# Kernel optimization log

Measured on AMD Instinct MI355X. Metric: run time of the kernel, lower is better.

Reference implementation:

```python
import jax, jax.numpy as jnp
import numpy as np

N, IN_DIM, HID = 8192, 256, 512
NEG_INF = jnp.float32(-1e30)


def _linear_params(key, fan_in, fan_out):
    k1, k2 = jax.random.split(key)
    bound = 1.0 / np.sqrt(fan_in)
    W = jax.random.uniform(k1, (fan_in, fan_out), jnp.float32, -bound, bound)
    b = jax.random.uniform(k2, (fan_out,), jnp.float32, -bound, bound)
    return W, b


def setup_inputs() -> dict:
    key = jax.random.key(0)
    ks = jax.random.split(key, 10)
    x = jax.random.normal(ks[0], (N, IN_DIM), jnp.float32)
    adj = jax.random.randint(ks[1], (N, N), 0, 2) > 0
    adj = adj | jnp.eye(N, dtype=bool)  # self-loops: no all-masked rows
    Win, b_in = _linear_params(ks[2], IN_DIM, HID)
    Wq, bq = _linear_params(ks[3], HID, HID)
    Wk, bk = _linear_params(ks[4], HID, HID)
    Wv, bv = _linear_params(ks[5], HID, HID)
    Wo, bo = _linear_params(ks[6], HID, HID)
    Ws, bs = _linear_params(ks[7], HID, 1)
    Wf1, bf1 = _linear_params(ks[8], HID, HID)
    Wf2, bf2 = _linear_params(ks[9], HID, HID)
    g1 = jnp.ones((HID,), jnp.float32); be1 = jnp.zeros((HID,), jnp.float32)
    g2 = jnp.ones((HID,), jnp.float32); be2 = jnp.zeros((HID,), jnp.float32)
    return dict(x=x, adj=adj, Win=Win, b_in=b_in, Wq=Wq, bq=bq, Wk=Wk, bk=bk,
                Wv=Wv, bv=bv, Wo=Wo, bo=bo, Ws=Ws, bs=bs,
                g1=g1, be1=be1, g2=g2, be2=be2,
                Wf1=Wf1, bf1=bf1, Wf2=Wf2, bf2=bf2)


def _layernorm(x, g, b, eps=1e-5):
    mu = jnp.mean(x, axis=-1, keepdims=True)
    var = jnp.mean(jnp.square(x - mu), axis=-1, keepdims=True)
    return (x - mu) * jax.lax.rsqrt(var + eps) * g + b


def reference(x, adj, Win, b_in, Wq, bq, Wk, bk, Wv, bv, Wo, bo, Ws, bs,
              g1, be1, g2, be2, Wf1, bf1, Wf2, bf2):
    h = x @ Win + b_in                      # [N, HID]
    q = h @ Wq + bq
    k = h @ Wk + bk
    v = h @ Wv + bv
    scale = 1.0 / np.sqrt(HID).astype(np.float32)
    scores = (q @ k.T) * scale              # [N, N]
    scores = jnp.where(adj, scores, NEG_INF)
    attn = jax.nn.softmax(scores, axis=-1)  # dropout = identity (eval mode)
    h2 = attn @ v                           # [N, HID]
    h = _layernorm(h + (h2 @ Wo + bo), g1, be1)
    ff = jnp.maximum(h @ Wf1 + bf1, 0.0) @ Wf2 + bf2
    h = _layernorm(h + ff, g2, be2)
    logits = (h @ Ws + bs).squeeze(-1)      # [N]
    return logits
```

## Files before the change

### kernel.cpp

```cpp
#include <hip/hip_runtime.h>

typedef unsigned int u32;
typedef unsigned short u16;
typedef unsigned char u8;

typedef __bf16 bf16_t;
typedef bf16_t bf16x8 __attribute__((ext_vector_type(8)));
typedef float f32x4 __attribute__((ext_vector_type(4)));

#define NROW 8192
#define HID 512
#define DIN 256
#define LDQ 1536
#define NSPLIT 4
#define KVCH (NROW / NSPLIT)
#define KVB 32

__device__ __forceinline__ u16 f2b(float f) {
    u32 u = __float_as_uint(f);
    u32 r = (u + 0x7fffu + ((u >> 16) & 1u)) >> 16;
    return (u16)r;
}
__device__ __forceinline__ float b2f(u16 h) {
    return __uint_as_float(((u32)h) << 16);
}
__device__ __forceinline__ f32x4 zero4() {
    f32x4 z = {0.f, 0.f, 0.f, 0.f};
    return z;
}
__device__ __forceinline__ void gll16(const void* g, void* l) {
    __builtin_amdgcn_global_load_lds(
        (const __attribute__((address_space(1))) unsigned int*)g,
        (__attribute__((address_space(3))) unsigned int*)l, 16, 0, 0);
}

__global__ void sniff_and_bias(const u32* __restrict__ adj, int* __restrict__ mode,
                               const float* __restrict__ bq, const float* __restrict__ bk,
                               const float* __restrict__ bv, float* __restrict__ bqkv) {
    __shared__ int f01[4], ff32[4], fbf[4];
    int t = threadIdx.x, lane = t & 63, wv = t >> 6;
    for (int i = t; i < 1536; i += 256)
        bqkv[i] = i < 512 ? bq[i] : (i < 1024 ? bk[i - 512] : bv[i - 1024]);
    int all01 = 1, allf32 = 1, allbf = 1;
    for (int i = t; i < 1024; i += 256) {
        u32 w = adj[i];
        if (w > 1u) all01 = 0;
        if (w != 0u && w != 0x3f800000u) allf32 = 0;
    }
    const u16* h = (const u16*)adj;
    for (int i = t; i < 2048; i += 256) {
        u16 v = h[i];
        if (v != 0 && v != 0x3f80u) allbf = 0;
    }
    all01 = __all(all01);
    allf32 = __all(allf32);
    allbf = __all(allbf);
    if (lane == 0) { f01[wv] = all01; ff32[wv] = allf32; fbf[wv] = allbf; }
    __syncthreads();
    if (t == 0) {
        int a = f01[0] & f01[1] & f01[2] & f01[3];
        int b = ff32[0] & ff32[1] & ff32[2] & ff32[3];
        int c = fbf[0] & fbf[1] & fbf[2] & fbf[3];
        mode[0] = a ? 0 : (b ? 1 : (c ? 2 : 3));
    }
}

__global__ __launch_bounds__(256) void build_bits(const void* __restrict__ adj,
                                                  const int* __restrict__ mode,
                                                  u32* __restrict__ bits) {
    int row = blockIdx.x;
    int t = threadIdx.x;
    int lane = t & 63, wv = t >> 6;
    int md = *mode;
    for (int c0 = 0; c0 < NROW; c0 += 256) {
        int c = c0 + t;
        size_t idx = (size_t)row * NROW + c;
        bool nz;
        if (md == 0)      nz = ((const u32*)adj)[idx] != 0u;
        else if (md == 1) nz = ((const float*)adj)[idx] != 0.f;
        else if (md == 2) nz = ((const u16*)adj)[idx] != 0;
        else              nz = ((const u8*)adj)[idx] != 0;
        unsigned long long bm = __ballot(nz);
        if (lane == 0) {
            int w = row * 256 + (c0 >> 5) + wv * 2;
            bits[w] = (u32)bm;
            bits[w + 1] = (u32)(bm >> 32);
        }
    }
}

__global__ __launch_bounds__(256) void prep(const float* __restrict__ x,
                                            const float* __restrict__ Win,
                                            const float* __restrict__ Wq,
                                            const float* __restrict__ Wk,
                                            const float* __restrict__ Wv,
                                            const float* __restrict__ Wo,
                                            const float* __restrict__ Wf1,
                                            const float* __restrict__ Wf2,
                                            u16* __restrict__ pX16,
                                            u16* __restrict__ pWinT,
                                            u16* __restrict__ pQKVT,
                                            u16* __restrict__ pWoT,
                                            u16* __restrict__ pWf1T,
                                            u16* __restrict__ pWf2T) {
    int z = blockIdx.z;
    int t = threadIdx.x;
    if (z == 7) {
        size_t base = ((size_t)blockIdx.y * 8 + blockIdx.x) * 32768;
#pragma unroll 4
        for (int k = 0; k < 128; k++) {
            size_t i = base + k * 256 + t;
            pX16[i] = f2b(x[i]);
        }
        return;
    }
    const float* src;
    u16* dst;
    int R = 512;
    switch (z) {
        case 0: src = Win; dst = pWinT; R = 256; break;
        case 1: src = Wq;  dst = pQKVT; break;
        case 2: src = Wk;  dst = pQKVT + 512 * 512; break;
        case 3: src = Wv;  dst = pQKVT + 2 * 512 * 512; break;
        case 4: src = Wo;  dst = pWoT; break;
        case 5: src = Wf1; dst = pWf1T; break;
        default: src = Wf2; dst = pWf2T; break;
    }
    int r0 = blockIdx.y * 64, c0 = blockIdx.x * 64;
    if (r0 >= R) return;
    __shared__ u16 tile[64][65];
#pragma unroll
    for (int i = 0; i < 16; i++) {
        int idx = t + i * 256;
        int rr = idx >> 6, cc = idx & 63;
        tile[rr][cc] = f2b(src[(size_t)(r0 + rr) * 512 + c0 + cc]);
    }
    __syncthreads();
#pragma unroll
    for (int i = 0; i < 16; i++) {
        int idx = t + i * 256;
        int rr = idx >> 6, cc = idx & 63;
        dst[(size_t)(c0 + rr) * R + r0 + cc] = tile[cc][rr];
    }
}

__global__ __launch_bounds__(256) void transpose_v_tiled(const u16* __restrict__ in, int ldv,
                                                         u16* __restrict__ out) {
    __shared__ u16 tl[64][72];
    int c0 = blockIdx.x * 64;
    int r0 = blockIdx.y * 64;
    int t = threadIdx.x;
#pragma unroll
    for (int i = 0; i < 2; i++) {
        int idx = t + i * 256;
        int rr = idx >> 3, ck = idx & 7;
        bf16x8 v = *(const bf16x8*)(in + (size_t)(r0 + rr) * ldv + c0 + ck * 8);
#pragma unroll
        for (int j = 0; j < 8; j++) tl[ck * 8 + j][rr] = ((u16*)&v)[j];
    }
    __syncthreads();
#pragma unroll
    for (int i = 0; i < 2; i++) {
        int idx = t + i * 256;
        int col = idx >> 3, ch = idx & 7;
        int kv = ch * 8;
        bf16x8 v;
#pragma unroll
        for (int j = 0; j < 8; j++) ((u16*)&v)[j] = tl[col][kv + j];
        *(bf16x8*)(out + (size_t)((r0 + kv) >> 5) * (HID * 32) +
                   (size_t)(c0 + col) * 32 + (kv & 31)) = v;
    }
}

__global__ __launch_bounds__(256, 3) void gemm_k(const u16* __restrict__ A, int lda,
                                                 const u16* __restrict__ Bt,
                                                 const float* __restrict__ bias,
                                                 const float* __restrict__ resid,
                                                 float* __restrict__ outF,
                                                 u16* __restrict__ outH, int ldo,
                                                 int relu, int K) {
    __shared__ u16 Ald[2][8192];
    __shared__ u16 Bld[2][4096];
    int t = threadIdx.x;
    int lane = t & 63, wave = t >> 6;
    int l15 = lane & 15, lg = lane >> 4;
    int row0 = blockIdx.y * 128, col0 = blockIdx.x * 64;

    auto stage = [&](int buf, int kk) {
#pragma unroll
        for (int p = 0; p < 4; p++) {
            int idx = p * 256 + t;
            int row = idx >> 3, c = idx & 7;
            gll16(A + (size_t)(row0 + row) * lda + kk + ((c ^ (row & 7)) * 8),
                  &Ald[buf][idx * 8]);
        }
#pragma unroll
        for (int p = 0; p < 2; p++) {
            int idx = p * 256 + t;
            int row = idx >> 3, c = idx & 7;
            gll16(Bt + (size_t)(col0 + row) * K + kk + ((c ^ (row & 7)) * 8),
                  &Bld[buf][idx * 8]);
        }
    };

    f32x4 acc[2][4];
#pragma unroll
    for (int i = 0; i < 2; i++)
#pragma unroll
        for (int j = 0; j < 4; j++) acc[i][j] = zero4();

    stage(0, 0);
    asm volatile("s_waitcnt vmcnt(0)" ::: "memory");
    __syncthreads();

    int nk = K >> 6;
    for (int kt = 0; kt < nk; kt++) {
        int buf = kt & 1;
        if (kt + 1 < nk) stage(buf ^ 1, (kt + 1) * 64);
#pragma unroll
        for (int ks = 0; ks < 2; ks++) {
            bf16x8 af[2], bfr[4];
#pragma unroll
            for (int i = 0; i < 2; i++) {
                int row = wave * 32 + i * 16 + l15;
                af[i] = *(const bf16x8*)&Ald[buf][row * 64 + (((ks * 4 + lg) ^ (row & 7)) * 8)];
            }
#pragma unroll
            for (int j = 0; j < 4; j++) {
                int row = j * 16 + l15;
                bfr[j] = *(const bf16x8*)&Bld[buf][row * 64 + (((ks * 4 + lg) ^ (row & 7)) * 8)];
            }
            __builtin_amdgcn_s_setprio(1);
#pragma unroll
            for (int i = 0; i < 2; i++)
#pragma unroll
                for (int j = 0; j < 4; j++)
                    acc[i][j] = __builtin_amdgcn_mfma_f32_16x16x32_bf16(af[i], bfr[j],
                                                                       acc[i][j], 0, 0, 0);
            __builtin_amdgcn_s_setprio(0);
        }
        asm volatile("s_waitcnt vmcnt(0)" ::: "memory");
        __syncthreads();
    }
#pragma unroll
    for (int j = 0; j < 4; j++) {
        int col = col0 + j * 16 + l15;
        float bv = bias[col];
#pragma unroll
        for (int i = 0; i < 2; i++) {
#pragma unroll
            for (int r = 0; r < 4; r++) {
                int row = row0 + wave * 32 + i * 16 + lg * 4 + r;
                float v = acc[i][j][r] + bv;
                if (relu) v = fmaxf(v, 0.f);
                size_t o = (size_t)row * ldo + col;
                if (resid) v += resid[o];
                if (outF) outF[o] = v;
                if (outH) outH[o] = f2b(v);
            }
        }
    }
}

__global__ __launch_bounds__(256, 2) void attn_kernel(const u16* __restrict__ QKV,
                                                      const u16* __restrict__ VTt,
                                                      const u32* __restrict__ bits,
                                                      u16* __restrict__ Opart,
                                                      float* __restrict__ Mpart,
                                                      float* __restrict__ Lpart) {
    extern __shared__ char smem[];
    u16* Klds = (u16*)smem;
    u16* Plds = (u16*)(smem + 65536);
    float* cscL = (float*)(smem + 69632);
    int* flagsL = (int*)(smem + 69888);
    int lane = threadIdx.x & 63, wave = threadIdx.x >> 6;
    int l15 = lane & 15, lg = lane >> 4;
    int s = blockIdx.x & 3;
    int qb = blockIdx.x >> 2;
    int qrow0 = qb * 64;
    int myrows = qrow0 + wave * 16;
    const u16* Kg = QKV + 512;

    bf16x8 qf[16];
    {
        const u16* qp = QKV + (size_t)(myrows + l15) * LDQ + lg * 8;
#pragma unroll
        for (int ks = 0; ks < 16; ks++) qf[ks] = *(const bf16x8*)(qp + ks * 32);
    }

    f32x4 acc[4][8];
#pragma unroll
    for (int i = 0; i < 4; i++)
#pragma unroll
        for (int j = 0; j < 8; j++) acc[i][j] = zero4();
    float m[4] = {-1e30f, -1e30f, -1e30f, -1e30f};
    float lsum[4] = {0.f, 0.f, 0.f, 0.f};
    const float scale = 0.04419417382415922f;
    int kvbeg = s * KVCH;

    auto STAGE = [&](int buf, int kv0) {
#pragma unroll
        for (int i = 0; i < 8; i++) {
            int seg = wave * 8 + i;
            int ks = seg >> 1, q = seg & 1;
            gll16(Kg + (size_t)(kv0 + q * 16 + l15) * LDQ + ks * 32 + lg * 8,
                  Klds + buf * 16384 + seg * 512 + lane * 8);
        }
    };

    STAGE(0, kvbeg);
    asm volatile("s_waitcnt vmcnt(0)" ::: "memory");
    __syncthreads();

    const int NT = KVCH / KVB;
    for (int t = 0; t < NT; ++t) {
        int kv0 = kvbeg + t * KVB;
        int buf = t & 1;
        const u16* kb = Klds + buf * 16384;

        f32x4 sf[2];
        sf[0] = zero4(); sf[1] = zero4();
        __builtin_amdgcn_s_setprio(1);
#pragma unroll
        for (int ks = 0; ks < 16; ks++) {
            bf16x8 b0 = *(const bf16x8*)(kb + (ks * 2) * 512 + lane * 8);
            bf16x8 b1 = *(const bf16x8*)(kb + (ks * 2 + 1) * 512 + lane * 8);
            sf[0] = __builtin_amdgcn_mfma_f32_16x16x32_bf16(qf[ks], b0, sf[0], 0, 0, 0);
            sf[1] = __builtin_amdgcn_mfma_f32_16x16x32_bf16(qf[ks], b1, sf[1], 0, 0, 0);
        }
        __builtin_amdgcn_s_setprio(0);

        u32 w0[4];
#pragma unroll
        for (int r = 0; r < 4; r++)
            w0[r] = bits[(size_t)(myrows + lg * 4 + r) * 256 + (kv0 >> 5)];
        float pvv[2][4];
        float mx[4] = {-1e30f, -1e30f, -1e30f, -1e30f};
#pragma unroll
        for (int f = 0; f < 2; f++) {
            int c = f * 16 + l15;
#pragma unroll
            for (int r = 0; r < 4; r++) {
                bool bit = (w0[r] >> c) & 1u;
                float sv = bit ? sf[f][r] * scale : -1e30f;
                pvv[f][r] = sv;
                mx[r] = fmaxf(mx[r], sv);
            }
        }
        bool need = false;
#pragma unroll
        for (int r = 0; r < 4; r++) need |= (mx[r] > m[r] + 8.0f);
        int wneed = __any(need ? 1 : 0);
        float cscv[4] = {1.f, 1.f, 1.f, 1.f};
        if (wneed) {
#pragma unroll
            for (int r = 0; r < 4; r++) {
#pragma unroll
                for (int off = 8; off; off >>= 1)
                    mx[r] = fmaxf(mx[r], __shfl_xor(mx[r], off, 64));
                float mn = fmaxf(m[r], mx[r]);
                cscv[r] = __expf(m[r] - mn);
                m[r] = mn;
                lsum[r] *= cscv[r];
            }
        }
        if (l15 == 0) *(f32x4*)&cscL[wave * 16 + lg * 4] = *(f32x4*)cscv;
        if (lane == 0) flagsL[wave] = wneed;

#pragma unroll
        for (int f = 0; f < 2; f++)
#pragma unroll
            for (int r = 0; r < 4; r++)
                pvv[f][r] = (pvv[f][r] < -1e29f) ? 0.f : __expf(pvv[f][r] - m[r]);
#pragma unroll
        for (int r = 0; r < 4; r++)
            lsum[r] += pvv[0][r] + pvv[1][r];

#pragma unroll
        for (int f = 0; f < 2; f++)
#pragma unroll
            for (int r = 0; r < 4; r++)
                Plds[wave * 512 + (f * 2 + (l15 >> 3)) * 128 + (lg * 4 + r) * 8 + (l15 & 7)] =
                    f2b(pvv[f][r]);

        asm volatile("s_waitcnt lgkmcnt(0)" ::: "memory");
        __builtin_amdgcn_sched_barrier(0);
        __builtin_amdgcn_s_barrier();
        __builtin_amdgcn_sched_barrier(0);

        if (t + 1 < NT) STAGE(buf ^ 1, kv0 + KVB);

        int anyf = __any(flagsL[lane & 3] != 0);
        if (anyf) {
#pragma unroll
            for (int rf = 0; rf < 4; rf++) {
                f32x4 cs = *(const f32x4*)&cscL[rf * 16 + lg * 4];
#pragma unroll
                for (int cf = 0; cf < 8; cf++) {
                    f32x4 a = acc[rf][cf];
                    a[0] *= cs[0]; a[1] *= cs[1]; a[2] *= cs[2]; a[3] *= cs[3];
                    acc[rf][cf] = a;
                }
            }
        }

#pragma unroll
        for (int g2 = 0; g2 < 2; g2++) {
            const u16* vb = VTt + (size_t)(kv0 >> 5) * (HID * 32) +
                            (size_t)(wave * 128 + g2 * 64) * 32;
            bf16x8 vv[4];
#pragma unroll
            for (int c4 = 0; c4 < 4; c4++)
                vv[c4] = *(const bf16x8*)(vb + (size_t)(c4 * 16 + l15) * 32 + lg * 8);
            __builtin_amdgcn_s_setprio(1);
#pragma unroll
            for (int rf = 0; rf < 4; rf++) {
                bf16x8 pa = *(const bf16x8*)(Plds + rf * 512 + lane * 8);
#pragma unroll
                for (int c4 = 0; c4 < 4; c4++)
                    acc[rf][g2 * 4 + c4] = __builtin_amdgcn_mfma_f32_16x16x32_bf16(
                        pa, vv[c4], acc[rf][g2 * 4 + c4], 0, 0, 0);
            }
            __builtin_amdgcn_s_setprio(0);
        }

        asm volatile("s_waitcnt vmcnt(0) lgkmcnt(0)" ::: "memory");
        __builtin_amdgcn_sched_barrier(0);
        __builtin_amdgcn_s_barrier();
        __builtin_amdgcn_sched_barrier(0);
    }

#pragma unroll
    for (int r = 0; r < 4; r++) {
#pragma unroll
        for (int off = 8; off; off >>= 1)
            lsum[r] += __shfl_xor(lsum[r], off, 64);
    }
    if (l15 == 0) {
#pragma unroll
        for (int r = 0; r < 4; r++) {
            size_t o = (size_t)s * NROW + myrows + lg * 4 + r;
            Mpart[o] = m[r];
            Lpart[o] = lsum[r];
        }
    }
#pragma unroll
    for (int rf = 0; rf < 4; rf++)
#pragma unroll
        for (int cf = 0; cf < 8; cf++) {
            int col = wave * 128 + cf * 16 + l15;
#pragma unroll
            for (int j = 0; j < 4; j++) {
                size_t row = (size_t)s * NROW + qrow0 + rf * 16 + lg * 4 + j;
                Opart[row * HID + col] = f2b(acc[rf][cf][j]);
            }
        }
}

__global__ __launch_bounds__(256) void attn_combine(const u16* __restrict__ Opart,
                                                    const float* __restrict__ Mpart,
                                                    const float* __restrict__ Lpart,
                                                    u16* __restrict__ O16) {
    int idx = blockIdx.x * 256 + threadIdx.x;
    int row = idx >> 6;
    int c8 = (idx & 63) << 3;
    float ms[NSPLIT], M = -1e30f;
#pragma unroll
    for (int s = 0; s < NSPLIT; s++) {
        ms[s] = Mpart[(size_t)s * NROW + row];
        M = fmaxf(M, ms[s]);
    }
    float w[NSPLIT], L = 0.f;
#pragma unroll
    for (int s = 0; s < NSPLIT; s++) {
        w[s] = __expf(ms[s] - M);
        L += Lpart[(size_t)s * NROW + row] * w[s];
    }
    float inv = 1.f / L;
    float o[8];
#pragma unroll
    for (int j = 0; j < 8; j++) o[j] = 0.f;
#pragma unroll
    for (int s = 0; s < NSPLIT; s++) {
        bf16x8 p = *(const bf16x8*)(Opart + ((size_t)s * NROW + row) * HID + c8);
#pragma unroll
        for (int j = 0; j < 8; j++) o[j] += (float)p[j] * w[s];
    }
    bf16x8 res;
#pragma unroll
    for (int j = 0; j < 8; j++) {
        u16 b = f2b(o[j] * inv);
        res[j] = *(bf16_t*)&b;
    }
    *(bf16x8*)(O16 + (size_t)row * HID + c8) = res;
}

__global__ __launch_bounds__(256) void ln_single(const float* __restrict__ a,
                                                 const float* __restrict__ g,
                                                 const float* __restrict__ be,
                                                 float* __restrict__ outF,
                                                 u16* __restrict__ outH) {
    int row = blockIdx.x, t = threadIdx.x;
    const float* ar = a + (size_t)row * HID;
    float x0 = ar[t];
    float x1 = ar[t + 256];
    float s = x0 + x1, s2 = x0 * x0 + x1 * x1;
#pragma unroll
    for (int off = 32; off; off >>= 1) {
        s += __shfl_xor(s, off, 64);
        s2 += __shfl_xor(s2, off, 64);
    }
    __shared__ float ls[4], ls2[4];
    int wv = t >> 6, ln = t & 63;
    if (ln == 0) { ls[wv] = s; ls2[wv] = s2; }
    __syncthreads();
    float S = ls[0] + ls[1] + ls[2] + ls[3];
    float S2 = ls2[0] + ls2[1] + ls2[2] + ls2[3];
    float mu = S * (1.f / 512.f);
    float var = S2 * (1.f / 512.f) - mu * mu;
    float inv = rsqrtf(var + 1e-5f);
    float y0 = (x0 - mu) * inv * g[t] + be[t];
    float y1 = (x1 - mu) * inv * g[t + 256] + be[t + 256];
    size_t o = (size_t)row * HID + t;
    outF[o] = y0; outF[o + 256] = y1;
    outH[o] = f2b(y0); outH[o + 256] = f2b(y1);
}

__global__ __launch_bounds__(256) void ln_logits(const float* __restrict__ a,
                                                 const float* __restrict__ g,
                                                 const float* __restrict__ be,
                                                 const float* __restrict__ Ws,
                                                 const float* __restrict__ bs,
                                                 float* __restrict__ out) {
    int row = blockIdx.x, t = threadIdx.x;
    const float* ar = a + (size_t)row * HID;
    float x0 = ar[t];
    float x1 = ar[t + 256];
    float s = x0 + x1, s2 = x0 * x0 + x1 * x1;
#pragma unroll
    for (int off = 32; off; off >>= 1) {
        s += __shfl_xor(s, off, 64);
        s2 += __shfl_xor(s2, off, 64);
    }
    __shared__ float ls[4], ls2[4], lp[4];
    int wv = t >> 6, ln = t & 63;
    if (ln == 0) { ls[wv] = s; ls2[wv] = s2; }
    __syncthreads();
    float S = ls[0] + ls[1] + ls[2] + ls[3];
    float S2 = ls2[0] + ls2[1] + ls2[2] + ls2[3];
    float mu = S * (1.f / 512.f);
    float var = S2 * (1.f / 512.f) - mu * mu;
    float inv = rsqrtf(var + 1e-5f);
    float y0 = (x0 - mu) * inv * g[t] + be[t];
    float y1 = (x1 - mu) * inv * g[t + 256] + be[t + 256];
    float p = y0 * Ws[t] + y1 * Ws[t + 256];
#pragma unroll
    for (int off = 32; off; off >>= 1) p += __shfl_xor(p, off, 64);
    if (ln == 0) lp[wv] = p;
    __syncthreads();
    if (t == 0) out[row] = lp[0] + lp[1] + lp[2] + lp[3] + bs[0];
}

extern "C" void kernel_launch(void* const* d_in, const int* in_sizes, int n_in,
                              void* d_out, int out_size, void* d_ws, size_t ws_size,
                              hipStream_t stream) {
    const float* x   = (const float*)d_in[0];
    const void*  adj = d_in[1];
    const float* Win = (const float*)d_in[2];
    const float* b_in= (const float*)d_in[3];
    const float* Wq  = (const float*)d_in[4];
    const float* bq  = (const float*)d_in[5];
    const float* Wk  = (const float*)d_in[6];
    const float* bk  = (const float*)d_in[7];
    const float* Wv  = (const float*)d_in[8];
    const float* bv  = (const float*)d_in[9];
    const float* Wo  = (const float*)d_in[10];
    const float* bo  = (const float*)d_in[11];
    const float* Ws  = (const float*)d_in[12];
    const float* bs  = (const float*)d_in[13];
    const float* g1  = (const float*)d_in[14];
    const float* be1 = (const float*)d_in[15];
    const float* g2  = (const float*)d_in[16];
    const float* be2 = (const float*)d_in[17];
    const float* Wf1 = (const float*)d_in[18];
    const float* bf1 = (const float*)d_in[19];
    const float* Wf2 = (const float*)d_in[20];
    const float* bf2 = (const float*)d_in[21];

    char* ws = (char*)d_ws;
    const size_t MB = 1u << 20;
    const size_t OFF_PART = 0;
    const size_t OFF_X16  = 0;
    const size_t OFF_H16  = 4 * MB;
    const size_t OFF_HN32 = 12 * MB;
    const size_t OFF_HN16 = 28 * MB;
    const size_t OFF_FF1  = 4 * MB;
    const size_t OFF_HF32 = 36 * MB;
    const size_t OFF_QKV  = 52 * MB;
    const size_t OFF_OP32 = 52 * MB;
    const size_t OFF_FF2  = 52 * MB;
    const size_t OFF_VT   = 76 * MB;
    const size_t OFF_H2   = 84 * MB;
    const size_t OFF_BITS = 92 * MB;
    size_t off = 100 * MB;
    const size_t OFF_WINT = off;  off += 262144;
    const size_t OFF_QKVT = off;  off += 1572864;
    const size_t OFF_WOT  = off;  off += 524288;
    const size_t OFF_WF1T = off;  off += 524288;
    const size_t OFF_WF2T = off;  off += 524288;
    const size_t OFF_BQKV = off;  off += 8192;
    const size_t OFF_MODE = off;  off += 4096;
    const size_t OFF_MPART= off;  off += 131072;
    const size_t OFF_LPART= off;  off += 131072;

    u16* pX16   = (u16*)(ws + OFF_X16);
    u16* pH16   = (u16*)(ws + OFF_H16);
    float* pHN32= (float*)(ws + OFF_HN32);
    u16* pHN16  = (u16*)(ws + OFF_HN16);
    u16* pFF1   = (u16*)(ws + OFF_FF1);
    float* pHF32= (float*)(ws + OFF_HF32);
    u16* pQKV   = (u16*)(ws + OFF_QKV);
    float* pOP32= (float*)(ws + OFF_OP32);
    float* pFF2 = (float*)(ws + OFF_FF2);
    u16* pVT    = (u16*)(ws + OFF_VT);
    u16* pH2    = (u16*)(ws + OFF_H2);
    u32* pBits  = (u32*)(ws + OFF_BITS);
    u16* pPart  = (u16*)(ws + OFF_PART);
    u16* pWinT  = (u16*)(ws + OFF_WINT);
    u16* pQKVT  = (u16*)(ws + OFF_QKVT);
    u16* pWoT   = (u16*)(ws + OFF_WOT);
    u16* pWf1T  = (u16*)(ws + OFF_WF1T);
    u16* pWf2T  = (u16*)(ws + OFF_WF2T);
    float* pBqkv= (float*)(ws + OFF_BQKV);
    int* pMode  = (int*)(ws + OFF_MODE);
    float* pMp  = (float*)(ws + OFF_MPART);
    float* pLp  = (float*)(ws + OFF_LPART);

    sniff_and_bias<<<1, 256, 0, stream>>>((const u32*)adj, pMode, bq, bk, bv, pBqkv);
    build_bits<<<NROW, 256, 0, stream>>>(adj, pMode, pBits);

    prep<<<dim3(8, 8, 8), 256, 0, stream>>>(x, Win, Wq, Wk, Wv, Wo, Wf1, Wf2,
                                            pX16, pWinT, pQKVT, pWoT, pWf1T, pWf2T);

    gemm_k<<<dim3(8, 64), 256, 0, stream>>>(pX16, DIN, pWinT, b_in, nullptr,
                                            pHF32, pH16, HID, 0, DIN);
    gemm_k<<<dim3(24, 64), 256, 0, stream>>>(pH16, HID, pQKVT, pBqkv, nullptr,
                                             nullptr, pQKV, LDQ, 0, HID);
    transpose_v_tiled<<<dim3(HID / 64, NROW / 64), 256, 0, stream>>>(pQKV + 1024, LDQ, pVT);
    attn_kernel<<<128 * NSPLIT, 256, 69920, stream>>>(pQKV, pVT, pBits, pPart, pMp, pLp);
    attn_combine<<<NROW * HID / (256 * 8), 256, 0, stream>>>(pPart, pMp, pLp, pH2);
    gemm_k<<<dim3(8, 64), 256, 0, stream>>>(pH2, HID, pWoT, bo, pHF32,
                                            pOP32, nullptr, HID, 0, HID);
    ln_single<<<NROW, 256, 0, stream>>>(pOP32, g1, be1, pHN32, pHN16);
    gemm_k<<<dim3(8, 64), 256, 0, stream>>>(pHN16, HID, pWf1T, bf1, nullptr,
                                            nullptr, pFF1, HID, 1, HID);
    gemm_k<<<dim3(8, 64), 256, 0, stream>>>(pFF1, HID, pWf2T, bf2, pHN32,
                                            pFF2, nullptr, HID, 0, HID);
    ln_logits<<<NROW, 256, 0, stream>>>(pFF2, g2, be2, Ws, bs, (float*)d_out);
}
```

Before: 517.6 us.

## Enlarge attention blocks to 8 waves with triple-buffered K and double-buffered P

The attention kernel now runs 512-thread blocks covering 128 query rows, with each wave owning 64 output columns instead of 128. K tiles are triple-buffered and prefetched two iterations ahead, and P and the rescale factors are double-buffered. This removes the second barrier per iteration and lets global loads overlap compute. In exchange it needs much more shared memory (about 113 KB), launches half as many blocks (256), and raises register pressure from holding Q fragments plus the accumulators.

```diff
diff --git a/kernel.cpp b/kernel.cpp
--- a/kernel.cpp
+++ b/kernel.cpp
@@ -262,7 +262,7 @@
     }
 }
 
-__global__ __launch_bounds__(256, 2) void attn_kernel(const u16* __restrict__ QKV,
+__global__ __launch_bounds__(512, 2) void attn_kernel(const u16* __restrict__ QKV,
                                                       const u16* __restrict__ VTt,
                                                       const u32* __restrict__ bits,
                                                       u16* __restrict__ Opart,
@@ -270,14 +270,14 @@
                                                       float* __restrict__ Lpart) {
     extern __shared__ char smem[];
     u16* Klds = (u16*)smem;
-    u16* Plds = (u16*)(smem + 65536);
-    float* cscL = (float*)(smem + 69632);
-    int* flagsL = (int*)(smem + 69888);
+    u16* Plds = (u16*)(smem + 98304);
+    float* cscL = (float*)(smem + 114688);
+    int* flagsL = (int*)(smem + 115712);
     int lane = threadIdx.x & 63, wave = threadIdx.x >> 6;
     int l15 = lane & 15, lg = lane >> 4;
     int s = blockIdx.x & 3;
     int qb = blockIdx.x >> 2;
-    int qrow0 = qb * 64;
+    int qrow0 = qb * 128;
     int myrows = qrow0 + wave * 16;
     const u16* Kg = QKV + 512;
 
@@ -288,11 +288,11 @@
         for (int ks = 0; ks < 16; ks++) qf[ks] = *(const bf16x8*)(qp + ks * 32);
     }
 
-    f32x4 acc[4][8];
-#pragma unroll
-    for (int i = 0; i < 4; i++)
-#pragma unroll
-        for (int j = 0; j < 8; j++) acc[i][j] = zero4();
+    f32x4 acc[8][4];
+#pragma unroll
+    for (int i = 0; i < 8; i++)
+#pragma unroll
+        for (int j = 0; j < 4; j++) acc[i][j] = zero4();
     float m[4] = {-1e30f, -1e30f, -1e30f, -1e30f};
     float lsum[4] = {0.f, 0.f, 0.f, 0.f};
     const float scale = 0.04419417382415922f;
@@ -300,8 +300,8 @@
 
     auto STAGE = [&](int buf, int kv0) {
 #pragma unroll
-        for (int i = 0; i < 8; i++) {
-            int seg = wave * 8 + i;
+        for (int i = 0; i < 4; i++) {
+            int seg = wave * 4 + i;
             int ks = seg >> 1, q = seg & 1;
             gll16(Kg + (size_t)(kv0 + q * 16 + l15) * LDQ + ks * 32 + lg * 8,
                   Klds + buf * 16384 + seg * 512 + lane * 8);
@@ -309,14 +309,17 @@
     };
 
     STAGE(0, kvbeg);
-    asm volatile("s_waitcnt vmcnt(0)" ::: "memory");
-    __syncthreads();
+    STAGE(1, kvbeg + KVB);
+    asm volatile("s_waitcnt vmcnt(4)" ::: "memory");
+    __builtin_amdgcn_sched_barrier(0);
+    __builtin_amdgcn_s_barrier();
+    __builtin_amdgcn_sched_barrier(0);
 
     const int NT = KVCH / KVB;
     for (int t = 0; t < NT; ++t) {
         int kv0 = kvbeg + t * KVB;
-        int buf = t & 1;
-        const u16* kb = Klds + buf * 16384;
+        const u16* kb = Klds + (t % 3) * 16384;
+        int pb = t & 1;
 
         f32x4 sf[2];
         sf[0] = zero4(); sf[1] = zero4();
@@ -364,8 +367,8 @@
                 lsum[r] *= cscv[r];
             }
         }
-        if (l15 == 0) *(f32x4*)&cscL[wave * 16 + lg * 4] = *(f32x4*)cscv;
-        if (lane == 0) flagsL[wave] = wneed;
+        if (l15 == 0) *(f32x4*)&cscL[pb * 128 + wave * 16 + lg * 4] = *(f32x4*)cscv;
+        if (lane == 0) flagsL[pb * 8 + wave] = wneed;
 
 #pragma unroll
         for (int f = 0; f < 2; f++)
@@ -380,23 +383,33 @@
         for (int f = 0; f < 2; f++)
 #pragma unroll
             for (int r = 0; r < 4; r++)
-                Plds[wave * 512 + (f * 2 + (l15 >> 3)) * 128 + (lg * 4 + r) * 8 + (l15 & 7)] =
-                    f2b(pvv[f][r]);
-
+                Plds[pb * 4096 + wave * 512 + (f * 2 + (l15 >> 3)) * 128 +
+                     (lg * 4 + r) * 8 + (l15 & 7)] = f2b(pvv[f][r]);
+
+        const u16* vb = VTt + (size_t)(kv0 >> 5) * (HID * 32) + (size_t)(wave * 64) * 32;
+        bf16x8 vv[4];
+#pragma unroll
+        for (int c4 = 0; c4 < 4; c4++)
+            vv[c4] = *(const bf16x8*)(vb + (size_t)(c4 * 16 + l15) * 32 + lg * 8);
+
+        if (t + 2 < NT) {
+            STAGE((t + 2) % 3, kv0 + 2 * KVB);
+            asm volatile("s_waitcnt vmcnt(4)" ::: "memory");
+        } else if (t + 1 < NT) {
+            asm volatile("s_waitcnt vmcnt(0)" ::: "memory");
+        }
         asm volatile("s_waitcnt lgkmcnt(0)" ::: "memory");
         __builtin_amdgcn_sched_barrier(0);
         __builtin_amdgcn_s_barrier();
         __builtin_amdgcn_sched_barrier(0);
 
-        if (t + 1 < NT) STAGE(buf ^ 1, kv0 + KVB);
-
-        int anyf = __any(flagsL[lane & 3] != 0);
+        int anyf = __any(flagsL[pb * 8 + (lane & 7)] != 0);
         if (anyf) {
 #pragma unroll
-            for (int rf = 0; rf < 4; rf++) {
-                f32x4 cs = *(const f32x4*)&cscL[rf * 16 + lg * 4];
-#pragma unroll
-                for (int cf = 0; cf < 8; cf++) {
+            for (int rf = 0; rf < 8; rf++) {
+                f32x4 cs = *(const f32x4*)&cscL[pb * 128 + rf * 16 + lg * 4];
+#pragma unroll
+                for (int cf = 0; cf < 4; cf++) {
                     f32x4 a = acc[rf][cf];
                     a[0] *= cs[0]; a[1] *= cs[1]; a[2] *= cs[2]; a[3] *= cs[3];
                     acc[rf][cf] = a;
@@ -404,30 +417,16 @@
             }
         }
 
-#pragma unroll
-        for (int g2 = 0; g2 < 2; g2++) {
-            const u16* vb = VTt + (size_t)(kv0 >> 5) * (HID * 32) +
-                            (size_t)(wave * 128 + g2 * 64) * 32;
-            bf16x8 vv[4];
-#pragma unroll
-            for (int c4 = 0; c4 < 4; c4++)
-                vv[c4] = *(const bf16x8*)(vb + (size_t)(c4 * 16 + l15) * 32 + lg * 8);
-            __builtin_amdgcn_s_setprio(1);
-#pragma unroll
-            for (int rf = 0; rf < 4; rf++) {
-                bf16x8 pa = *(const bf16x8*)(Plds + rf * 512 + lane * 8);
-#pragma unroll
-                for (int c4 = 0; c4 < 4; c4++)
-                    acc[rf][g2 * 4 + c4] = __builtin_amdgcn_mfma_f32_16x16x32_bf16(
-                        pa, vv[c4], acc[rf][g2 * 4 + c4], 0, 0, 0);
-            }
-            __builtin_amdgcn_s_setprio(0);
-        }
-
-        asm volatile("s_waitcnt vmcnt(0) lgkmcnt(0)" ::: "memory");
-        __builtin_amdgcn_sched_barrier(0);
-        __builtin_amdgcn_s_barrier();
-        __builtin_amdgcn_sched_barrier(0);
+        __builtin_amdgcn_s_setprio(1);
+#pragma unroll
+        for (int rf = 0; rf < 8; rf++) {
+            bf16x8 pa = *(const bf16x8*)(Plds + pb * 4096 + rf * 512 + lane * 8);
+#pragma unroll
+            for (int cf = 0; cf < 4; cf++)
+                acc[rf][cf] = __builtin_amdgcn_mfma_f32_16x16x32_bf16(pa, vv[cf],
+                                                                     acc[rf][cf], 0, 0, 0);
+        }
+        __builtin_amdgcn_s_setprio(0);
     }
 
 #pragma unroll
@@ -445,10 +444,10 @@
         }
     }
 #pragma unroll
-    for (int rf = 0; rf < 4; rf++)
-#pragma unroll
-        for (int cf = 0; cf < 8; cf++) {
-            int col = wave * 128 + cf * 16 + l15;
+    for (int rf = 0; rf < 8; rf++)
+#pragma unroll
+        for (int cf = 0; cf < 4; cf++) {
+            int col = wave * 64 + cf * 16 + l15;
 #pragma unroll
             for (int j = 0; j < 4; j++) {
                 size_t row = (size_t)s * NROW + qrow0 + rf * 16 + lg * 4 + j;
@@ -647,7 +646,7 @@
     gemm_k<<<dim3(24, 64), 256, 0, stream>>>(pH16, HID, pQKVT, pBqkv, nullptr,
                                              nullptr, pQKV, LDQ, 0, HID);
     transpose_v_tiled<<<dim3(HID / 64, NROW / 64), 256, 0, stream>>>(pQKV + 1024, LDQ, pVT);
-    attn_kernel<<<128 * NSPLIT, 256, 69920, stream>>>(pQKV, pVT, pBits, pPart, pMp, pLp);
+    attn_kernel<<<64 * NSPLIT, 512, 115776, stream>>>(pQKV, pVT, pBits, pPart, pMp, pLp);
     attn_combine<<<NROW * HID / (256 * 8), 256, 0, stream>>>(pPart, pMp, pLp, pH2);
     gemm_k<<<dim3(8, 64), 256, 0, stream>>>(pH2, HID, pWoT, bo, pHF32,
                                             pOP32, nullptr, HID, 0, HID);
```

After: 486.5 us (median of 2 runs). -6.0%, faster.
